# Performance work log

Hardware: AMD Instinct MI355X
Metric: run time of the kernel (lower is better)

## Reference

```python
import jax, jax.numpy as jnp
import numpy as np

N_NODES = 50000
N_EDGES = 800000
HID = 128


def setup_inputs() -> dict:
    key = jax.random.key(0)
    ks = jax.random.split(key, 10)
    s_msg = 1.0 / np.sqrt(2 * HID + 1)
    s_u1 = 1.0 / np.sqrt(2 * HID)
    s_u2 = 1.0 / np.sqrt(HID)
    return {
        "z": jax.random.normal(ks[0], (N_NODES, HID), dtype=jnp.float32),
        "edge_weight": jax.random.uniform(ks[1], (N_EDGES,), dtype=jnp.float32),
        "edge_src": jax.random.randint(ks[2], (N_EDGES,), 0, N_NODES),
        "edge_dst": jax.random.randint(ks[3], (N_EDGES,), 0, N_NODES),
        "Wm": jax.random.normal(ks[4], (2 * HID + 1, HID), dtype=jnp.float32) * s_msg,
        "bm": jax.random.normal(ks[5], (HID,), dtype=jnp.float32) * s_msg,
        "W1": jax.random.normal(ks[6], (2 * HID, HID), dtype=jnp.float32) * s_u1,
        "b1": jax.random.normal(ks[7], (HID,), dtype=jnp.float32) * s_u1,
        "W2": jax.random.normal(ks[8], (HID, HID), dtype=jnp.float32) * s_u2,
        "b2": jax.random.normal(ks[9], (HID,), dtype=jnp.float32) * s_u2,
    }


def reference(z, edge_weight, edge_src, edge_dst, Wm, bm, W1, b1, W2, b2):
    n, H = z.shape
    # message Linear on concat([z[u], z[v], w]) split to avoid materializing [E, 2H+1]
    Wd, Ws, ww = Wm[:H], Wm[H:2 * H], Wm[2 * H]  # [H,H], [H,H], [H]
    msgs = (z[edge_dst] @ Wd + z[edge_src] @ Ws
            + edge_weight[:, None] * ww[None, :] + bm)  # [E, H]
    # max-aggregate messages per destination node; zeros for isolated nodes
    agg = jax.ops.segment_max(msgs, edge_dst, num_segments=n)  # [n, H], -inf if empty
    deg = jax.ops.segment_sum(jnp.ones_like(edge_weight), edge_dst, num_segments=n)
    agg = jnp.where(deg[:, None] > 0, agg, jnp.zeros((), dtype=z.dtype))
    # update MLP on concat([z, agg]) split into two GEMMs
    W1a, W1b = W1[:H], W1[H:]
    hidden = jax.nn.relu(z @ W1a + agg @ W1b + b1)  # [n, H]
    return hidden @ W2 + b2  # [n, H]
```

## Files before the change

### kernel.cpp

```cpp
#include <hip/hip_runtime.h>
#include <hip/hip_bf16.h>

#define HID 128

typedef short bf16x8 __attribute__((ext_vector_type(8)));
typedef float f32x4  __attribute__((ext_vector_type(4)));
typedef unsigned short u16;
typedef unsigned long long u64;

__device__ __forceinline__ u16 f2bf(float f) {
    __hip_bfloat16 h = __float2bfloat16(f);
    return *reinterpret_cast<u16*>(&h);
}
__device__ __forceinline__ float bf2f(u16 x) {
    unsigned u = ((unsigned)x) << 16;
    return __uint_as_float(u);
}
__device__ __forceinline__ u64 pack_rec(int dst, int src, float w) {
    int wq = (int)fmaf(w, 32768.f, 0.5f);
    wq = wq > 32767 ? 32767 : wq;
    return ((u64)(unsigned)dst << 31) | ((unsigned)src << 15) | (unsigned)wq;
}


__global__ __launch_bounds__(256)
void prep_hist(const float* __restrict__ z, const float* __restrict__ Wm,
               const float* __restrict__ W1, const float* __restrict__ W2,
               const int* __restrict__ edst,
               u16* __restrict__ Ab, u16* __restrict__ Wt, int* __restrict__ bhist,
               int N, int Mp, int E, int bz, int bw, int nbk)
{
    __shared__ int lh[256];
    const int b = blockIdx.x;
    const int t = threadIdx.x;
    if (b < bz) {
        const int idx4 = (b * 256 + t) * 4;
        if (idx4 >= Mp * 128) return;
        const int row = idx4 >> 7, col = idx4 & 127;
        ushort4 u;
        if (row < N) {
            const float4 v = *(const float4*)&z[(size_t)row * 128 + col];
            u.x = f2bf(v.x); u.y = f2bf(v.y); u.z = f2bf(v.z); u.w = f2bf(v.w);
        } else { u.x = 0; u.y = 0; u.z = 0; u.w = 0; }
        *(ushort4*)&Ab[(size_t)row * 256 + col] = u;
    } else if (b < bz + bw) {
        const int idx = (b - bz) * 256 + t;
        if (idx >= 81920) return;
        float v;
        if (idx < 32768) {
            const int nn = idx >> 7, k = idx & 127;
            v = (nn < 128) ? Wm[k * 128 + nn] : Wm[(128 + k) * 128 + (nn - 128)];
        } else if (idx < 65536) {
            const int j = idx - 32768, n = j >> 8, k = j & 255;
            v = W1[k * 128 + n];
        } else {
            const int j = idx - 65536, n = j >> 7, k = j & 127;
            v = W2[k * 128 + n];
        }
        Wt[idx] = f2bf(v);
    } else {
        lh[t] = 0;
        __syncthreads();
        const int e0 = (b - bz - bw) * 4096;
        const int eend = min(e0 + 4096, E);
        for (int e = e0 + t; e < eend; e += 256)
            atomicAdd(&lh[edst[e] >> 8], 1);
        __syncthreads();
        if (t < nbk && lh[t] > 0) atomicAdd(&bhist[t], lh[t]);
    }
}

__global__ __launch_bounds__(256)
void scatter_gemmP(const int* __restrict__ esrc, const int* __restrict__ edst,
                   const float* __restrict__ ew,
                   const int* __restrict__ bhist, int* __restrict__ brun,
                   u64* __restrict__ tmp, int E, int nbk, int nsc,
                   const u16* __restrict__ Ab, const u16* __restrict__ Wds_t,
                   u16* __restrict__ Pb, int Mp)
{
    __shared__ int cnt[256];
    __shared__ int rbase[256];
    __shared__ int bbase[256];
    __shared__ u16 As[64 * 136];
    const int t = threadIdx.x;

    if (blockIdx.x < nsc) {
        const int e0 = blockIdx.x * 4096;
        const int eend = min(e0 + 4096, E);

        cnt[t] = 0;
        if (t == 0) {
            int run = 0;
            for (int i = 0; i < nbk; i++) { bbase[i] = run; run += bhist[i]; }
        }
        __syncthreads();

        if (eend - e0 == 4096) {
            int myb[16]; u64 myrec[16];
#pragma unroll
            for (int i = 0; i < 16; i++) {
                const int e = e0 + t + i * 256;
                const int d = edst[e];
                myb[i] = d >> 8;
                myrec[i] = pack_rec(d, esrc[e], ew[e]);
                atomicAdd(&cnt[myb[i]], 1);
            }
            __syncthreads();
            if (t < nbk && cnt[t] > 0) rbase[t] = bbase[t] + atomicAdd(&brun[t], cnt[t]);
            __syncthreads();
            cnt[t] = 0;
            __syncthreads();
#pragma unroll
            for (int i = 0; i < 16; i++) {
                const int r = atomicAdd(&cnt[myb[i]], 1);
                tmp[(size_t)rbase[myb[i]] + r] = myrec[i];
            }
        } else {
            for (int e = e0 + t; e < eend; e += 256)
                atomicAdd(&cnt[edst[e] >> 8], 1);
            __syncthreads();
            if (t < nbk && cnt[t] > 0) rbase[t] = bbase[t] + atomicAdd(&brun[t], cnt[t]);
            __syncthreads();
            cnt[t] = 0;
            __syncthreads();
            for (int e = e0 + t; e < eend; e += 256) {
                const int d = edst[e];
                const int bk = d >> 8;
                const int r = atomicAdd(&cnt[bk], 1);
                tmp[(size_t)rbase[bk] + r] = pack_rec(d, esrc[e], ew[e]);
            }
        }
    } else {
        const int row0 = (blockIdx.x - nsc) * 64;
        const int wv = t >> 6, lane = t & 63;
        const int wy = wv & 1, wx = wv >> 1;
        const int q = lane >> 4, n = lane & 15;

#pragma unroll
        for (int i = 0; i < 4; i++) {
            const int chunk = i * 256 + t;
            const int row = chunk >> 4;
            const int c8 = chunk & 15;
            *(bf16x8*)&As[row * 136 + c8 * 8] =
                *(const bf16x8*)&Ab[(size_t)(row0 + row) * 256 + c8 * 8];
        }
        __syncthreads();

        const u16* pAl = As + (wy * 32 + n) * 136 + q * 8;
        const u16* pB = Wds_t + (size_t)(wx * 128 + n) * 128 + q * 8;

        f32x4 acc[2][8];
#pragma unroll
        for (int i = 0; i < 2; i++)
#pragma unroll
            for (int j = 0; j < 8; j++) acc[i][j] = f32x4{0.f, 0.f, 0.f, 0.f};

#pragma unroll
        for (int kk = 0; kk < 128; kk += 32) {
            bf16x8 a0 = *(const bf16x8*)(pAl + kk);
            bf16x8 a1 = *(const bf16x8*)(pAl + 16 * 136 + kk);
            bf16x8 bfr[8];
#pragma unroll
            for (int ni = 0; ni < 8; ni++)
                bfr[ni] = *(const bf16x8*)(pB + (size_t)ni * 16 * 128 + kk);
#pragma unroll
            for (int ni = 0; ni < 8; ni++) {
                acc[0][ni] = __builtin_amdgcn_mfma_f32_16x16x32_bf16(a0, bfr[ni], acc[0][ni], 0, 0, 0);
                acc[1][ni] = __builtin_amdgcn_mfma_f32_16x16x32_bf16(a1, bfr[ni], acc[1][ni], 0, 0, 0);
            }
        }

#pragma unroll
        for (int mi = 0; mi < 2; mi++) {
#pragma unroll
            for (int ni = 0; ni < 8; ni++) {
                const int rbase2 = row0 + wy * 32 + mi * 16 + q * 4;
                const int c = wx * 128 + ni * 16 + n;
#pragma unroll
                for (int r = 0; r < 4; r++)
                    Pb[(size_t)(rbase2 + r) * 256 + c] = f2bf(acc[mi][ni][r]);
            }
        }
    }
}

__global__ __launch_bounds__(256)
void bucket_sort(const u64* __restrict__ tmp, const int* __restrict__ bhist,
                 int* __restrict__ offsets, unsigned* __restrict__ s_ew,
                 int N, int E, int nbk)
{
    __shared__ int cnt[256];
    __shared__ int cur[256];
    __shared__ int ps[256];
    __shared__ int sh_base[2];
    const int b = blockIdx.x;
    const int t = threadIdx.x;
    const int n0 = b << 8;
    const int nhi = min(256, N - n0);

    if (t == 0) {
        int run = 0;
        for (int i = 0; i < b; i++) run += bhist[i];
        sh_base[0] = run;
        sh_base[1] = run + bhist[b];
    }
    cnt[t] = 0;
    __syncthreads();
    const int base = sh_base[0];
    const int endp = sh_base[1];

    for (int r = base + t; r < endp; r += 256)
        atomicAdd(&cnt[(int)(tmp[r] >> 31) - n0], 1);
    __syncthreads();

    const int v = cnt[t];
    ps[t] = v;
    __syncthreads();
    for (int off = 1; off < 256; off <<= 1) {
        int add = (t >= off) ? ps[t - off] : 0;
        __syncthreads();
        ps[t] += add;
        __syncthreads();
    }
    cur[t] = base + ps[t] - v;
    __syncthreads();

    if (t < nhi) offsets[n0 + t] = cur[t];
    if (t == 0 && n0 + nhi == N) offsets[N] = E;

    for (int r = base + t; r < endp; r += 256) {
        const u64 rec = tmp[r];
        const int local = (int)(rec >> 31) - n0;
        const int pos = atomicAdd(&cur[local], 1);
        s_ew[pos] = (unsigned)(rec & 0x7FFFFFFFu);
    }
}

__global__ __launch_bounds__(256)
void aggregate_kernel(const u16* __restrict__ Pb,
                      const float* __restrict__ bm,
                      const float* __restrict__ ww,
                      const int* __restrict__ offsets,
                      const unsigned* __restrict__ s_ew,
                      u16* __restrict__ Ab, int N, int Mp)
{
    const int t = threadIdx.x;
    const int lane = t & 63;
    const int c0 = (lane & 15) * 8;
    const int nd = blockIdx.x * 16 + ((t >> 6) << 2) + (lane >> 4);
    if (nd >= Mp) return;

    u16* dst = &Ab[(size_t)nd * 256 + 128 + c0];

    int start = 0, end = 0;
    if (nd < N) { start = offsets[nd]; end = offsets[nd + 1]; }

    if (end <= start) {
        bf16x8 zv = {0, 0, 0, 0, 0, 0, 0, 0};
        *(bf16x8*)dst = zv;
        return;
    }

    float wwv[8];
    {
        const float4 wa = *(const float4*)&ww[c0];
        const float4 wb = *(const float4*)&ww[c0 + 4];
        wwv[0] = wa.x; wwv[1] = wa.y; wwv[2] = wa.z; wwv[3] = wa.w;
        wwv[4] = wb.x; wwv[5] = wb.y; wwv[6] = wb.z; wwv[7] = wb.w;
    }

    const float kq = 1.f / 32768.f;
    float m[8];
#pragma unroll
    for (int j = 0; j < 8; j++) m[j] = -INFINITY;

    const int last = end - 1;
    for (int eb = start; eb < end; eb += 8) {
        unsigned u[8];
#pragma unroll
        for (int i = 0; i < 8; i++) {
            int e = eb + i; if (e > last) e = last;
            u[i] = s_ew[e];
        }
        bf16x8 p[8];
#pragma unroll
        for (int i = 0; i < 8; i++)
            p[i] = *(const bf16x8*)&Pb[(size_t)(u[i] >> 15) * 256 + 128 + c0];
#pragma unroll
        for (int i = 0; i < 8; i++) {
            const float w = (float)(u[i] & 32767u) * kq;
#pragma unroll
            for (int j = 0; j < 8; j++)
                m[j] = fmaxf(m[j], fmaf(w, wwv[j], bf2f((u16)p[i][j])));
        }
    }

    const bf16x8 zd = *(const bf16x8*)&Pb[(size_t)nd * 256 + c0];
    float bmv[8];
    {
        const float4 ba = *(const float4*)&bm[c0];
        const float4 bb = *(const float4*)&bm[c0 + 4];
        bmv[0] = ba.x; bmv[1] = ba.y; bmv[2] = ba.z; bmv[3] = ba.w;
        bmv[4] = bb.x; bmv[5] = bb.y; bmv[6] = bb.z; bmv[7] = bb.w;
    }
    bf16x8 outv;
#pragma unroll
    for (int j = 0; j < 8; j++)
        outv[j] = (short)f2bf(bf2f((u16)zd[j]) + bmv[j] + m[j]);
    *(bf16x8*)dst = outv;
}

__global__ __launch_bounds__(256)
void gemm_HO(const u16* __restrict__ Ab, const u16* __restrict__ W1t,
             const float* __restrict__ b1, const u16* __restrict__ W2t,
             const float* __restrict__ b2, float* __restrict__ out, int Mstore)
{
    __shared__ u16 smem[64 * 264];

    const int row0 = blockIdx.x * 64;
    const int tid = threadIdx.x;
    const int wv = tid >> 6, lane = tid & 63;
    const int wy = wv & 1, wx = wv >> 1;
    const int q = lane >> 4, n = lane & 15;

#pragma unroll
    for (int i = 0; i < 8; i++) {
        const int chunk = i * 256 + tid;
        const int row = chunk >> 5;
        const int c8 = chunk & 31;
        *(bf16x8*)&smem[row * 264 + c8 * 8] =
            *(const bf16x8*)&Ab[(size_t)(row0 + row) * 256 + c8 * 8];
    }
    __syncthreads();

    f32x4 acc[2][4];

    {
        const u16* pAl = smem + (wy * 32 + n) * 264 + q * 8;
        const u16* pB = W1t + (size_t)(wx * 64 + n) * 256 + q * 8;

#pragma unroll
        for (int i = 0; i < 2; i++)
#pragma unroll
            for (int j = 0; j < 4; j++) acc[i][j] = f32x4{0.f, 0.f, 0.f, 0.f};

#pragma unroll
        for (int kk = 0; kk < 256; kk += 32) {
            bf16x8 b0 = *(const bf16x8*)(pB + kk);
            bf16x8 b1f = *(const bf16x8*)(pB + 16 * 256 + kk);
            bf16x8 b2f = *(const bf16x8*)(pB + 32 * 256 + kk);
            bf16x8 b3f = *(const bf16x8*)(pB + 48 * 256 + kk);
            bf16x8 a0 = *(const bf16x8*)(pAl + kk);
            bf16x8 a1 = *(const bf16x8*)(pAl + 16 * 264 + kk);
            acc[0][0] = __builtin_amdgcn_mfma_f32_16x16x32_bf16(a0, b0,  acc[0][0], 0, 0, 0);
            acc[0][1] = __builtin_amdgcn_mfma_f32_16x16x32_bf16(a0, b1f, acc[0][1], 0, 0, 0);
            acc[0][2] = __builtin_amdgcn_mfma_f32_16x16x32_bf16(a0, b2f, acc[0][2], 0, 0, 0);
            acc[0][3] = __builtin_amdgcn_mfma_f32_16x16x32_bf16(a0, b3f, acc[0][3], 0, 0, 0);
            acc[1][0] = __builtin_amdgcn_mfma_f32_16x16x32_bf16(a1, b0,  acc[1][0], 0, 0, 0);
            acc[1][1] = __builtin_amdgcn_mfma_f32_16x16x32_bf16(a1, b1f, acc[1][1], 0, 0, 0);
            acc[1][2] = __builtin_amdgcn_mfma_f32_16x16x32_bf16(a1, b2f, acc[1][2], 0, 0, 0);
            acc[1][3] = __builtin_amdgcn_mfma_f32_16x16x32_bf16(a1, b3f, acc[1][3], 0, 0, 0);
        }
    }
    __syncthreads();

#pragma unroll
    for (int mi = 0; mi < 2; mi++) {
#pragma unroll
        for (int ni = 0; ni < 4; ni++) {
            const int rl = wy * 32 + mi * 16 + q * 4;
            const int c = wx * 64 + ni * 16 + n;
#pragma unroll
            for (int r = 0; r < 4; r++) {
                float v = acc[mi][ni][r] + b1[c];
                smem[(rl + r) * 136 + c] = f2bf(fmaxf(v, 0.f));
            }
        }
    }
    __syncthreads();

    {
        const u16* pB = W2t + (size_t)(wx * 64 + n) * 128 + q * 8;
        const u16* pHl = smem + (wy * 32 + n) * 136 + q * 8;

#pragma unroll
        for (int i = 0; i < 2; i++)
#pragma unroll
            for (int j = 0; j < 4; j++) acc[i][j] = f32x4{0.f, 0.f, 0.f, 0.f};

#pragma unroll
        for (int kk = 0; kk < 128; kk += 32) {
            bf16x8 b0 = *(const bf16x8*)(pB + kk);
            bf16x8 b1f = *(const bf16x8*)(pB + 16 * 128 + kk);
            bf16x8 b2f = *(const bf16x8*)(pB + 32 * 128 + kk);
            bf16x8 b3f = *(const bf16x8*)(pB + 48 * 128 + kk);
            bf16x8 a0 = *(const bf16x8*)(pHl + kk);
            bf16x8 a1 = *(const bf16x8*)(pHl + 16 * 136 + kk);
            acc[0][0] = __builtin_amdgcn_mfma_f32_16x16x32_bf16(a0, b0,  acc[0][0], 0, 0, 0);
            acc[0][1] = __builtin_amdgcn_mfma_f32_16x16x32_bf16(a0, b1f, acc[0][1], 0, 0, 0);
            acc[0][2] = __builtin_amdgcn_mfma_f32_16x16x32_bf16(a0, b2f, acc[0][2], 0, 0, 0);
            acc[0][3] = __builtin_amdgcn_mfma_f32_16x16x32_bf16(a0, b3f, acc[0][3], 0, 0, 0);
            acc[1][0] = __builtin_amdgcn_mfma_f32_16x16x32_bf16(a1, b0,  acc[1][0], 0, 0, 0);
            acc[1][1] = __builtin_amdgcn_mfma_f32_16x16x32_bf16(a1, b1f, acc[1][1], 0, 0, 0);
            acc[1][2] = __builtin_amdgcn_mfma_f32_16x16x32_bf16(a1, b2f, acc[1][2], 0, 0, 0);
            acc[1][3] = __builtin_amdgcn_mfma_f32_16x16x32_bf16(a1, b3f, acc[1][3], 0, 0, 0);
        }

#pragma unroll
        for (int mi = 0; mi < 2; mi++) {
#pragma unroll
            for (int ni = 0; ni < 4; ni++) {
                const int rbase = row0 + wy * 32 + mi * 16 + q * 4;
                const int c = wx * 64 + ni * 16 + n;
#pragma unroll
                for (int r = 0; r < 4; r++) {
                    const int rr = rbase + r;
                    if (rr >= Mstore) continue;
                    out[(size_t)rr * 128 + c] = acc[mi][ni][r] + b2[c];
                }
            }
        }
    }
}

extern "C" void kernel_launch(void* const* d_in, const int* in_sizes, int n_in,
                              void* d_out, int out_size, void* d_ws, size_t ws_size,
                              hipStream_t stream) {
    const float* z    = (const float*)d_in[0];
    const float* ew   = (const float*)d_in[1];
    const int*   esrc = (const int*)d_in[2];
    const int*   edst = (const int*)d_in[3];
    const float* Wm   = (const float*)d_in[4];
    const float* bm   = (const float*)d_in[5];
    const float* W1   = (const float*)d_in[6];
    const float* b1   = (const float*)d_in[7];
    const float* W2   = (const float*)d_in[8];
    const float* b2   = (const float*)d_in[9];
    float* out = (float*)d_out;

    const int N  = in_sizes[0] / HID;
    const int E  = in_sizes[1];
    const int Mp = ((N + 63) / 64) * 64;
    const int nbk = (N + 255) / 256;

    char* w = (char*)d_ws;
    u16*  Ab      = (u16*)w;      w += (size_t)Mp * 256 * 2;
    u16*  Pb      = (u16*)w;      w += (size_t)Mp * 256 * 2;
    u16*  Wt      = (u16*)w;      w += (size_t)81920 * 2;
    int*  offsets = (int*)w;      w += (size_t)(N + 64) * 4;
    int*  bhist   = (int*)w;      w += 256 * 4;
    int*  brun    = (int*)w;      w += 256 * 4;
    unsigned* s_ew = (unsigned*)w; w += (size_t)E * 4;
    u64*  tmp     = (u64*)w;      w += (size_t)E * 8;

    const int bz = (Mp * 32 + 255) / 256;
    const int bw = (81920 + 255) / 256;
    const int bh = (E + 4095) / 4096;
    const int nsc = (E + 4095) / 4096;

    hipMemsetAsync(bhist, 0, 512 * sizeof(int), stream);
    prep_hist<<<bz + bw + bh, 256, 0, stream>>>(z, Wm, W1, W2, edst, Ab, Wt, bhist,
                                                N, Mp, E, bz, bw, nbk);
    scatter_gemmP<<<nsc + Mp / 64, 256, 0, stream>>>(esrc, edst, ew, bhist, brun,
                                                     tmp, E, nbk, nsc,
                                                     Ab, Wt, Pb, Mp);
    bucket_sort<<<nbk, 256, 0, stream>>>(tmp, bhist, offsets, s_ew, N, E, nbk);
    aggregate_kernel<<<(Mp + 15) / 16, 256, 0, stream>>>(Pb, bm, Wm + 256 * 128,
                                                         offsets, s_ew, Ab, N, Mp);
    gemm_HO<<<Mp / 64, 256, 0, stream>>>(Ab, Wt + 32768, b1, Wt + 65536, b2, out, N);
}
```

Measured before the change: 210.8 us.

## Regroup pipeline stages so scatter overlaps cast and sort overlaps GEMM

Splits the histogram into its own small kernel, then co-schedules the z/weight bf16 cast with the edge scatter, and the bucket sort with the P GEMM in one launch each. Bucket base offsets are now computed by a parallel shared-memory scan instead of a serial loop on thread 0. The cast is widened to 8 elements per thread. The intent is to fill the GPU with independent work at each stage and cut serial prefix-sum latency, at the cost of repeating the same scan in every block.

New measurement: 209.1 us. About the same (-0.8%).

```diff
diff --git a/kernel.cpp b/kernel.cpp
--- a/kernel.cpp
+++ b/kernel.cpp
@@ -24,28 +24,48 @@
 
 
 __global__ __launch_bounds__(256)
-void prep_hist(const float* __restrict__ z, const float* __restrict__ Wm,
-               const float* __restrict__ W1, const float* __restrict__ W2,
-               const int* __restrict__ edst,
-               u16* __restrict__ Ab, u16* __restrict__ Wt, int* __restrict__ bhist,
-               int N, int Mp, int E, int bz, int bw, int nbk)
+void hist_kernel(const int* __restrict__ edst, int* __restrict__ bhist,
+                 int E, int nbk)
 {
     __shared__ int lh[256];
     const int b = blockIdx.x;
     const int t = threadIdx.x;
+    lh[t] = 0;
+    __syncthreads();
+    const int e0 = b * 4096;
+    const int eend = min(e0 + 4096, E);
+    for (int e = e0 + t; e < eend; e += 256)
+        atomicAdd(&lh[edst[e] >> 8], 1);
+    __syncthreads();
+    if (t < nbk && lh[t] > 0) atomicAdd(&bhist[t], lh[t]);
+}
+
+__global__ __launch_bounds__(256)
+void cast_scatter(const float* __restrict__ z, const float* __restrict__ Wm,
+                  const float* __restrict__ W1, const float* __restrict__ W2,
+                  const int* __restrict__ esrc, const int* __restrict__ edst,
+                  const float* __restrict__ ew,
+                  const int* __restrict__ bhist, int* __restrict__ brun,
+                  u16* __restrict__ Ab, u16* __restrict__ Wt, u64* __restrict__ tmp,
+                  int N, int Mp, int E, int bz, int bw, int nbk)
+{
+    const int b = blockIdx.x;
+    const int t = threadIdx.x;
     if (b < bz) {
-        const int idx4 = (b * 256 + t) * 4;
-        if (idx4 >= Mp * 128) return;
-        const int row = idx4 >> 7, col = idx4 & 127;
-        ushort4 u;
+        const int idx8 = (b * 256 + t) * 8;
+        const int row = idx8 >> 7, col = idx8 & 127;
+        bf16x8 u;
         if (row < N) {
-            const float4 v = *(const float4*)&z[(size_t)row * 128 + col];
-            u.x = f2bf(v.x); u.y = f2bf(v.y); u.z = f2bf(v.z); u.w = f2bf(v.w);
-        } else { u.x = 0; u.y = 0; u.z = 0; u.w = 0; }
-        *(ushort4*)&Ab[(size_t)row * 256 + col] = u;
+            const float4 v0 = *(const float4*)&z[(size_t)row * 128 + col];
+            const float4 v1 = *(const float4*)&z[(size_t)row * 128 + col + 4];
+            u[0] = (short)f2bf(v0.x); u[1] = (short)f2bf(v0.y);
+            u[2] = (short)f2bf(v0.z); u[3] = (short)f2bf(v0.w);
+            u[4] = (short)f2bf(v1.x); u[5] = (short)f2bf(v1.y);
+            u[6] = (short)f2bf(v1.z); u[7] = (short)f2bf(v1.w);
+        } else { u = bf16x8{0,0,0,0,0,0,0,0}; }
+        *(bf16x8*)&Ab[(size_t)row * 256 + col] = u;
     } else if (b < bz + bw) {
         const int idx = (b - bz) * 256 + t;
-        if (idx >= 81920) return;
         float v;
         if (idx < 32768) {
             const int nn = idx >> 7, k = idx & 127;
@@ -59,40 +79,24 @@
         }
         Wt[idx] = f2bf(v);
     } else {
-        lh[t] = 0;
-        __syncthreads();
+        __shared__ int cnt[256];
+        __shared__ int rbase[256];
+        __shared__ int bbase[256];
+        __shared__ int ps[256];
         const int e0 = (b - bz - bw) * 4096;
         const int eend = min(e0 + 4096, E);
-        for (int e = e0 + t; e < eend; e += 256)
-            atomicAdd(&lh[edst[e] >> 8], 1);
-        __syncthreads();
-        if (t < nbk && lh[t] > 0) atomicAdd(&bhist[t], lh[t]);
-    }
-}
-
-__global__ __launch_bounds__(256)
-void scatter_gemmP(const int* __restrict__ esrc, const int* __restrict__ edst,
-                   const float* __restrict__ ew,
-                   const int* __restrict__ bhist, int* __restrict__ brun,
-                   u64* __restrict__ tmp, int E, int nbk, int nsc,
-                   const u16* __restrict__ Ab, const u16* __restrict__ Wds_t,
-                   u16* __restrict__ Pb, int Mp)
-{
-    __shared__ int cnt[256];
-    __shared__ int rbase[256];
-    __shared__ int bbase[256];
-    __shared__ u16 As[64 * 136];
-    const int t = threadIdx.x;
-
-    if (blockIdx.x < nsc) {
-        const int e0 = blockIdx.x * 4096;
-        const int eend = min(e0 + 4096, E);
-
+
+        const int h = (t < nbk) ? bhist[t] : 0;
+        ps[t] = h;
+        __syncthreads();
+        for (int off = 1; off < 256; off <<= 1) {
+            int add = (t >= off) ? ps[t - off] : 0;
+            __syncthreads();
+            ps[t] += add;
+            __syncthreads();
+        }
+        bbase[t] = ps[t] - h;
         cnt[t] = 0;
-        if (t == 0) {
-            int run = 0;
-            for (int i = 0; i < nbk; i++) { bbase[i] = run; run += bhist[i]; }
-        }
         __syncthreads();
 
         if (eend - e0 == 4096) {
@@ -130,8 +134,68 @@
                 tmp[(size_t)rbase[bk] + r] = pack_rec(d, esrc[e], ew[e]);
             }
         }
+    }
+}
+
+__global__ __launch_bounds__(256)
+void sort_gemmP(const u64* __restrict__ tmp, const int* __restrict__ bhist,
+                int* __restrict__ offsets, unsigned* __restrict__ s_ew,
+                int N, int E, int nbk,
+                const u16* __restrict__ Ab, const u16* __restrict__ Wds_t,
+                u16* __restrict__ Pb, int Mp)
+{
+    const int t = threadIdx.x;
+
+    if (blockIdx.x < (unsigned)nbk) {
+        __shared__ int cnt[256];
+        __shared__ int cur[256];
+        __shared__ int ps[256];
+        const int b = blockIdx.x;
+        const int n0 = b << 8;
+        const int nhi = min(256, N - n0);
+
+        const int h = (t < nbk) ? bhist[t] : 0;
+        ps[t] = h;
+        __syncthreads();
+        for (int off = 1; off < 256; off <<= 1) {
+            int add = (t >= off) ? ps[t - off] : 0;
+            __syncthreads();
+            ps[t] += add;
+            __syncthreads();
+        }
+        const int base = (b > 0) ? ps[b - 1] : 0;
+        const int endp = ps[b];
+        cnt[t] = 0;
+        __syncthreads();
+
+        for (int r = base + t; r < endp; r += 256)
+            atomicAdd(&cnt[(int)(tmp[r] >> 31) - n0], 1);
+        __syncthreads();
+
+        const int v = cnt[t];
+        ps[t] = v;
+        __syncthreads();
+        for (int off = 1; off < 256; off <<= 1) {
+            int add = (t >= off) ? ps[t - off] : 0;
+            __syncthreads();
+            ps[t] += add;
+            __syncthreads();
+        }
+        cur[t] = base + ps[t] - v;
+        __syncthreads();
+
+        if (t < nhi) offsets[n0 + t] = cur[t];
+        if (t == 0 && n0 + nhi == N) offsets[N] = E;
+
+        for (int r = base + t; r < endp; r += 256) {
+            const u64 rec = tmp[r];
+            const int local = (int)(rec >> 31) - n0;
+            const int pos = atomicAdd(&cur[local], 1);
+            s_ew[pos] = (unsigned)(rec & 0x7FFFFFFFu);
+        }
     } else {
-        const int row0 = (blockIdx.x - nsc) * 64;
+        __shared__ u16 As[64 * 136];
+        const int row0 = (blockIdx.x - nbk) * 64;
         const int wv = t >> 6, lane = t & 63;
         const int wy = wv & 1, wx = wv >> 1;
         const int q = lane >> 4, n = lane & 15;
@@ -181,58 +245,6 @@
                     Pb[(size_t)(rbase2 + r) * 256 + c] = f2bf(acc[mi][ni][r]);
             }
         }
-    }
-}
-
-__global__ __launch_bounds__(256)
-void bucket_sort(const u64* __restrict__ tmp, const int* __restrict__ bhist,
-                 int* __restrict__ offsets, unsigned* __restrict__ s_ew,
-                 int N, int E, int nbk)
-{
-    __shared__ int cnt[256];
-    __shared__ int cur[256];
-    __shared__ int ps[256];
-    __shared__ int sh_base[2];
-    const int b = blockIdx.x;
-    const int t = threadIdx.x;
-    const int n0 = b << 8;
-    const int nhi = min(256, N - n0);
-
-    if (t == 0) {
-        int run = 0;
-        for (int i = 0; i < b; i++) run += bhist[i];
-        sh_base[0] = run;
-        sh_base[1] = run + bhist[b];
-    }
-    cnt[t] = 0;
-    __syncthreads();
-    const int base = sh_base[0];
-    const int endp = sh_base[1];
-
-    for (int r = base + t; r < endp; r += 256)
-        atomicAdd(&cnt[(int)(tmp[r] >> 31) - n0], 1);
-    __syncthreads();
-
-    const int v = cnt[t];
-    ps[t] = v;
-    __syncthreads();
-    for (int off = 1; off < 256; off <<= 1) {
-        int add = (t >= off) ? ps[t - off] : 0;
-        __syncthreads();
-        ps[t] += add;
-        __syncthreads();
-    }
-    cur[t] = base + ps[t] - v;
-    __syncthreads();
-
-    if (t < nhi) offsets[n0 + t] = cur[t];
-    if (t == 0 && n0 + nhi == N) offsets[N] = E;
-
-    for (int r = base + t; r < endp; r += 256) {
-        const u64 rec = tmp[r];
-        const int local = (int)(rec >> 31) - n0;
-        const int pos = atomicAdd(&cur[local], 1);
-        s_ew[pos] = (unsigned)(rec & 0x7FFFFFFFu);
     }
 }
 
@@ -453,18 +465,17 @@
     unsigned* s_ew = (unsigned*)w; w += (size_t)E * 4;
     u64*  tmp     = (u64*)w;      w += (size_t)E * 8;
 
-    const int bz = (Mp * 32 + 255) / 256;
-    const int bw = (81920 + 255) / 256;
-    const int bh = (E + 4095) / 4096;
+    const int bz8 = (Mp * 16 + 255) / 256;
+    const int bw  = (81920 + 255) / 256;
     const int nsc = (E + 4095) / 4096;
 
     hipMemsetAsync(bhist, 0, 512 * sizeof(int), stream);
-    prep_hist<<<bz + bw + bh, 256, 0, stream>>>(z, Wm, W1, W2, edst, Ab, Wt, bhist,
-                                                N, Mp, E, bz, bw, nbk);
-    scatter_gemmP<<<nsc + Mp / 64, 256, 0, stream>>>(esrc, edst, ew, bhist, brun,
-                                                     tmp, E, nbk, nsc,
-                                                     Ab, Wt, Pb, Mp);
-    bucket_sort<<<nbk, 256, 0, stream>>>(tmp, bhist, offsets, s_ew, N, E, nbk);
+    hist_kernel<<<nsc, 256, 0, stream>>>(edst, bhist, E, nbk);
+    cast_scatter<<<bz8 + bw + nsc, 256, 0, stream>>>(z, Wm, W1, W2, esrc, edst, ew,
+                                                     bhist, brun, Ab, Wt, tmp,
+                                                     N, Mp, E, bz8, bw, nbk);
+    sort_gemmP<<<nbk + Mp / 64, 256, 0, stream>>>(tmp, bhist, offsets, s_ew,
+                                                  N, E, nbk, Ab, Wt, Pb, Mp);
     aggregate_kernel<<<(Mp + 15) / 16, 256, 0, stream>>>(Pb, bm, Wm + 256 * 128,
                                                          offsets, s_ew, Ab, N, Mp);
     gemm_HO<<<Mp / 64, 256, 0, stream>>>(Ab, Wt + 32768, b1, Wt + 65536, b2, out, N);
```
